# Performance work log

Measured on AMD Instinct MI355X. Metric: run time of the kernel, lower is better.

Reference implementation:

```python
import jax, jax.numpy as jnp
import numpy as np
from jax import lax

ANCHOR_BASE = np.array([
    [-37.254833, -82.50967, 53.254833, 98.50967],
    [-82.50967, -173.01933, 98.50967, 189.01933],
    [-173.01933, -354.03867, 189.01933, 370.03867],
    [-56.0, -56.0, 72.0, 72.0],
    [-120.0, -120.0, 136.0, 136.0],
    [-248.0, -248.0, 264.0, 264.0],
    [-82.50967, -37.254833, 98.50967, 53.254833],
    [-173.01933, -82.50967, 189.01933, 98.50967],
    [-354.03867, -173.01933, 370.03867, 189.01933]], dtype=np.float32)
FEAT_STRIDE = 16
IMG_H, IMG_W = 608, 800          # feature map 38x50 at stride 16
NMS_THRESH = 0.7
PRE_NMS, POST_NMS = 6000, 300
MIN_SIZE = 16.0                  # scale = 1.0


def setup_inputs() -> dict:
    key = jax.random.key(0)
    ks = jax.random.split(key, 7)
    H, W = 38, 50
    x = jax.random.normal(ks[0], (1, 512, H, W), jnp.float32)
    conv1_w = jax.random.normal(ks[1], (512, 512, 3, 3), jnp.float32) * 0.01
    conv1_b = jnp.zeros((512,), jnp.float32)
    loc_w = jax.random.normal(ks[2], (36, 512, 1, 1), jnp.float32) * 0.01
    loc_b = jnp.zeros((36,), jnp.float32)
    score_w = jax.random.normal(ks[3], (18, 512, 1, 1), jnp.float32) * 0.01
    score_b = jnp.zeros((18,), jnp.float32)
    return {"x": x, "conv1_w": conv1_w, "conv1_b": conv1_b,
            "loc_w": loc_w, "loc_b": loc_b,
            "score_w": score_w, "score_b": score_b}


def _conv(x, w, b, pad):
    y = lax.conv_general_dilated(x, w, (1, 1), pad,
                                 dimension_numbers=("NCHW", "OIHW", "NCHW"))
    return y + b[None, :, None, None]


def _make_anchors(h, w):
    ab = jnp.asarray(ANCHOR_BASE)                       # [A,4]
    yy = jnp.arange(h, dtype=jnp.float32) * FEAT_STRIDE
    xx = jnp.arange(w, dtype=jnp.float32) * FEAT_STRIDE
    sy, sx = jnp.meshgrid(yy, xx, indexing="ij")        # [h,w]
    shift = jnp.stack([sy, sx, sy, sx], axis=-1).reshape(-1, 4)  # [K,4]
    return (shift[:, None, :] + ab[None, :, :]).reshape(-1, 4)   # [K*A,4]


def _loc2bbox(anchor, loc):
    ah = anchor[:, 2] - anchor[:, 0]
    aw = anchor[:, 3] - anchor[:, 1]
    acy = anchor[:, 0] + 0.5 * ah
    acx = anchor[:, 1] + 0.5 * aw
    dy, dx, dh, dw = loc[:, 0], loc[:, 1], loc[:, 2], loc[:, 3]
    cy = dy * ah + acy
    cx = dx * aw + acx
    h = jnp.exp(dh) * ah
    w = jnp.exp(dw) * aw
    return jnp.stack([cy - 0.5 * h, cx - 0.5 * w,
                      cy + 0.5 * h, cx + 0.5 * w], axis=1)


def _iou_matrix(b):  # b: [K,4] (y1,x1,y2,x2)
    area = (b[:, 2] - b[:, 0]) * (b[:, 3] - b[:, 1])
    ty1 = jnp.maximum(b[:, None, 0], b[None, :, 0])
    tx1 = jnp.maximum(b[:, None, 1], b[None, :, 1])
    ty2 = jnp.minimum(b[:, None, 2], b[None, :, 2])
    tx2 = jnp.minimum(b[:, None, 3], b[None, :, 3])
    inter = jnp.clip(ty2 - ty1, 0) * jnp.clip(tx2 - tx1, 0)
    return inter / jnp.maximum(area[:, None] + area[None, :] - inter, 1e-9)


def _nms_keep(boxes, valid, thresh):
    # boxes already sorted by score desc; greedy suppression.
    K = boxes.shape[0]
    iou = _iou_matrix(boxes)                 # [K,K]
    idx = jnp.arange(K)

    def body(i, keep):
        sup = (iou[i] > thresh) & (idx > i) & keep[i]
        return keep & ~sup

    keep = lax.fori_loop(0, K, body, valid)
    return keep


def reference(x, conv1_w, conv1_b, loc_w, loc_b, score_w, score_b):
    H, W = x.shape[2], x.shape[3]
    A = ANCHOR_BASE.shape[0]

    h1 = jax.nn.relu(_conv(x, conv1_w, conv1_b, ((1, 1), (1, 1))))
    locs = _conv(h1, loc_w, loc_b, ((0, 0), (0, 0)))      # [1,36,H,W]
    scores = _conv(h1, score_w, score_b, ((0, 0), (0, 0)))  # [1,18,H,W]

    locs = locs.transpose(0, 2, 3, 1).reshape(-1, 4)        # [H*W*A,4]
    fg = scores.transpose(0, 2, 3, 1).reshape(H, W, A, 2)[..., 1].reshape(-1)

    anchor = _make_anchors(H, W)
    roi = _loc2bbox(anchor, locs)
    roi = jnp.stack([jnp.clip(roi[:, 0], 0, IMG_H),
                     jnp.clip(roi[:, 1], 0, IMG_W),
                     jnp.clip(roi[:, 2], 0, IMG_H),
                     jnp.clip(roi[:, 3], 0, IMG_W)], axis=1)

    hs = roi[:, 2] - roi[:, 0]
    ws = roi[:, 3] - roi[:, 1]
    valid = (hs >= MIN_SIZE) & (ws >= MIN_SIZE)
    score_f = jnp.where(valid, fg, -jnp.inf)

    top_scores, top_idx = lax.top_k(score_f, PRE_NMS)
    top_boxes = roi[top_idx]                                # [PRE_NMS,4]
    top_valid = top_scores > -jnp.inf

    keep = _nms_keep(top_boxes, top_valid, NMS_THRESH)

    # take first POST_NMS kept boxes into a fixed-shape output
    rank = jnp.cumsum(keep.astype(jnp.int32)) - 1
    dest = jnp.where(keep & (rank < POST_NMS), rank, POST_NMS)
    out = jnp.zeros((POST_NMS + 1, 4), top_boxes.dtype).at[dest].add(top_boxes)
    return out[:POST_NMS]
```

## Files before the change

### kernel.cpp

```cpp
#include <hip/hip_runtime.h>
#include <cstdint>
#include <cstddef>

typedef unsigned long long u64;

#define CIN   512
#define H     38
#define W     50
#define HW    1900
#define PH    40
#define PW    52
#define NA    17100
#define NSORT 32768
#define PRE   6000
#define POST  300
#define NW    94
#define MTS   6016

__constant__ float c_AB[36] = {
  -37.254833f,  -82.50967f,   53.254833f,  98.50967f,
  -82.50967f,  -173.01933f,   98.50967f,  189.01933f,
 -173.01933f,  -354.03867f,  189.01933f,  370.03867f,
  -56.f, -56.f, 72.f, 72.f,
 -120.f,-120.f,136.f,136.f,
 -248.f,-248.f,264.f,264.f,
  -82.50967f,  -37.254833f,   98.50967f,  53.254833f,
 -173.01933f,  -82.50967f,   189.01933f,  98.50967f,
 -354.03867f, -173.01933f,   370.03867f, 189.01933f
};

__global__ __launch_bounds__(256) void pad_kernel(const float* __restrict__ x, float* __restrict__ xp) {
  int idx = blockIdx.x * 256 + threadIdx.x;
  int c   = idx / (PH * PW);
  int rem = idx - c * (PH * PW);
  int yy  = rem / PW;
  int xx  = rem - yy * PW;
  float v = 0.f;
  if (yy >= 1 && yy <= H && xx >= 1 && xx <= W)
    v = x[(size_t)c * HW + (yy - 1) * W + (xx - 1)];
  xp[idx] = v;
}

__global__ __launch_bounds__(256) void wtrans_kernel(const float* __restrict__ w1, float* __restrict__ wt) {
  __shared__ float tile[9][16][17];
  int o0 = blockIdx.x * 16, i0 = blockIdx.y * 16;
  int tx = threadIdx.x & 15, ty = threadIdx.x >> 4;
  #pragma unroll
  for (int r = 0; r < 9; ++r)
    tile[r][tx][ty] = w1[((size_t)(o0 + ty) * CIN + (i0 + tx)) * 9 + r];
  __syncthreads();
  #pragma unroll
  for (int r = 0; r < 9; ++r)
    wt[((size_t)r * CIN + i0 + ty) * CIN + o0 + tx] = tile[r][ty][tx];
}

__global__ __launch_bounds__(256) void wt2prep_kernel(const float* __restrict__ lw, const float* __restrict__ sw,
                                                      float* __restrict__ wt2) {
  int t = blockIdx.x * 256 + threadIdx.x;
  int k = t >> 6, o = t & 63;
  float v = 0.f;
  if (o < 36)      v = lw[o * CIN + k];
  else if (o < 54) v = sw[(o - 36) * CIN + k];
  wt2[t] = v;
}

__global__ __launch_bounds__(256) void conv_gemm_kernel(const float* __restrict__ wt, const float* __restrict__ xp,
                                                        float* __restrict__ part) {
  __shared__ __align__(16) float As[16][64];
  __shared__ __align__(16) float Bs[16][64];
  const int tid   = threadIdx.x;
  const int obase = blockIdx.x * 64;
  const int pbase = blockIdx.y * 64;
  const int split = blockIdx.z;
  const int kbeg = split * 1536, kend = kbeg + 1536;
  const int krow = tid >> 4;
  const int c4   = (tid & 15) * 4;
  const int to   = (tid & 15) * 4;
  const int tp   = (tid >> 4) * 4;
  float acc[4][4] = {};
  float av[4], bv[4];

  auto loadAB = [&](int k0) {
    int k = k0 + krow;
    const float* ap = &wt[(size_t)k * CIN + obase + c4];
    av[0] = ap[0]; av[1] = ap[1]; av[2] = ap[2]; av[3] = ap[3];
    int r = k >> 9;
    int i = k & 511;
    int ky = r / 3, kx = r - ky * 3;
    const float* xpi = &xp[(size_t)i * (PH * PW)];
    #pragma unroll
    for (int j = 0; j < 4; ++j) {
      int p = pbase + c4 + j;
      float v = 0.f;
      if (p < HW) {
        int y = p / W, xx = p - y * W;
        v = xpi[(y + ky) * PW + xx + kx];
      }
      bv[j] = v;
    }
  };

  loadAB(kbeg);
  for (int k0 = kbeg; k0 < kend; k0 += 16) {
    __syncthreads();
    *(float4*)&As[krow][c4] = make_float4(av[0], av[1], av[2], av[3]);
    *(float4*)&Bs[krow][c4] = make_float4(bv[0], bv[1], bv[2], bv[3]);
    __syncthreads();
    if (k0 + 16 < kend) loadAB(k0 + 16);
    #pragma unroll
    for (int kk = 0; kk < 16; ++kk) {
      float4 a4 = *(const float4*)&As[kk][to];
      float4 b4 = *(const float4*)&Bs[kk][tp];
      float ar[4] = {a4.x, a4.y, a4.z, a4.w};
      float br[4] = {b4.x, b4.y, b4.z, b4.w};
      #pragma unroll
      for (int ii = 0; ii < 4; ++ii)
        #pragma unroll
        for (int jj = 0; jj < 4; ++jj)
          acc[ii][jj] += ar[ii] * br[jj];
    }
  }
  float* dst = part + (size_t)split * CIN * HW;
  #pragma unroll
  for (int ii = 0; ii < 4; ++ii) {
    int o = obase + to + ii;
    int p = pbase + tp;
    float* rowp = dst + (size_t)o * HW;
    if (p + 3 < HW) {
      *(float4*)&rowp[p] = make_float4(acc[ii][0], acc[ii][1], acc[ii][2], acc[ii][3]);
    } else {
      #pragma unroll
      for (int jj = 0; jj < 4; ++jj) if (p + jj < HW) rowp[p + jj] = acc[ii][jj];
    }
  }
}

__global__ __launch_bounds__(256) void reduce_relu_kernel(const float* __restrict__ part, const float* __restrict__ b1,
                                                          float* __restrict__ h1) {
  int idx = blockIdx.x * 256 + threadIdx.x;
  int o = idx / HW;
  float v = part[idx] + part[(size_t)CIN * HW + idx] + part[(size_t)2 * CIN * HW + idx] + b1[o];
  h1[idx] = v > 0.f ? v : 0.f;
}

__global__ __launch_bounds__(256) void heads_gemm_kernel(const float* __restrict__ wt2, const float* __restrict__ h1,
                                                         const float* __restrict__ lb, const float* __restrict__ sb,
                                                         float* __restrict__ c2) {
  __shared__ __align__(16) float As[16][64];
  __shared__ __align__(16) float Bs[16][64];
  const int tid   = threadIdx.x;
  const int pbase = blockIdx.x * 64;
  const int krow = tid >> 4;
  const int c4   = (tid & 15) * 4;
  const int to   = (tid & 15) * 4;
  const int tp   = (tid >> 4) * 4;
  float acc[4][4] = {};
  float av[4], bv[4];

  auto loadAB = [&](int k0) {
    int k = k0 + krow;
    const float4 a4 = *(const float4*)&wt2[k * 64 + c4];
    av[0] = a4.x; av[1] = a4.y; av[2] = a4.z; av[3] = a4.w;
    #pragma unroll
    for (int j = 0; j < 4; ++j) {
      int p = pbase + c4 + j;
      bv[j] = (p < HW) ? h1[(size_t)k * HW + p] : 0.f;
    }
  };

  loadAB(0);
  for (int k0 = 0; k0 < CIN; k0 += 16) {
    __syncthreads();
    *(float4*)&As[krow][c4] = make_float4(av[0], av[1], av[2], av[3]);
    *(float4*)&Bs[krow][c4] = make_float4(bv[0], bv[1], bv[2], bv[3]);
    __syncthreads();
    if (k0 + 16 < CIN) loadAB(k0 + 16);
    #pragma unroll
    for (int kk = 0; kk < 16; ++kk) {
      float4 a4 = *(const float4*)&As[kk][to];
      float4 b4 = *(const float4*)&Bs[kk][tp];
      float ar[4] = {a4.x, a4.y, a4.z, a4.w};
      float br[4] = {b4.x, b4.y, b4.z, b4.w};
      #pragma unroll
      for (int ii = 0; ii < 4; ++ii)
        #pragma unroll
        for (int jj = 0; jj < 4; ++jj)
          acc[ii][jj] += ar[ii] * br[jj];
    }
  }
  #pragma unroll
  for (int ii = 0; ii < 4; ++ii) {
    int o = to + ii;
    float bias = 0.f;
    if (o < 36) bias = lb[o]; else if (o < 54) bias = sb[o - 36];
    int p = pbase + tp;
    float* rowp = c2 + (size_t)o * HW;
    #pragma unroll
    for (int jj = 0; jj < 4; ++jj) if (p + jj < HW) rowp[p + jj] = acc[ii][jj] + bias;
  }
}

__global__ __launch_bounds__(256) void decode_kernel(const float* __restrict__ c2, float* __restrict__ roi,
                                                     u64* __restrict__ keys) {
  int n = blockIdx.x * 256 + threadIdx.x;
  if (n >= NSORT) return;
  if (n >= NA) { keys[n] = ~0ull; return; }
  unsigned p = (unsigned)n / 9u;
  unsigned a = (unsigned)n - p * 9u;
  unsigned y = p / 50u;
  unsigned x = p - y * 50u;
  float dy = c2[(a * 4 + 0) * HW + p];
  float dx = c2[(a * 4 + 1) * HW + p];
  float dh = c2[(a * 4 + 2) * HW + p];
  float dw = c2[(a * 4 + 3) * HW + p];
  float fg = c2[(37 + a * 2) * HW + p];
  float sy = (float)(y * 16u), sx = (float)(x * 16u);
  float ay1 = sy + c_AB[a * 4 + 0], ax1 = sx + c_AB[a * 4 + 1];
  float ay2 = sy + c_AB[a * 4 + 2], ax2 = sx + c_AB[a * 4 + 3];
  float ahh = ay2 - ay1, aww = ax2 - ax1;
  float acy = ay1 + 0.5f * ahh, acx = ax1 + 0.5f * aww;
  float cy = dy * ahh + acy, cx = dx * aww + acx;
  float hh = expf(dh) * ahh, ww = expf(dw) * aww;
  float y1 = cy - 0.5f * hh, x1 = cx - 0.5f * ww;
  float y2 = cy + 0.5f * hh, x2 = cx + 0.5f * ww;
  y1 = fminf(fmaxf(y1, 0.f), 608.f); x1 = fminf(fmaxf(x1, 0.f), 800.f);
  y2 = fminf(fmaxf(y2, 0.f), 608.f); x2 = fminf(fmaxf(x2, 0.f), 800.f);
  *(float4*)&roi[(size_t)n * 4] = make_float4(y1, x1, y2, x2);
  bool valid = ((y2 - y1) >= 16.f) && ((x2 - x1) >= 16.f);
  float sc = valid ? fg : -__builtin_huge_valf();
  unsigned m = __float_as_uint(sc);
  m = (m & 0x80000000u) ? ~m : (m | 0x80000000u);
  unsigned km = ~m;
  keys[n] = ((u64)km << 32) | (unsigned)n;
}

__global__ __launch_bounds__(1024) void sort_kernel(u64* __restrict__ keys) {
  __shared__ u64 s[8192];
  const int tid = threadIdx.x;
  u64* base = keys + (size_t)blockIdx.x * 8192;
  for (int i = tid; i < 8192; i += 1024) s[i] = base[i];
  __syncthreads();
  for (int k = 2; k <= 8192; k <<= 1) {
    for (int j = k >> 1; j > 0; j >>= 1) {
      for (int i = tid; i < 8192; i += 1024) {
        int l = i ^ j;
        if (l > i) {
          u64 xa = s[i], xb = s[l];
          bool up = ((i & k) == 0);
          if ((xa > xb) == up) { s[i] = xb; s[l] = xa; }
        }
      }
      __syncthreads();
    }
  }
  for (int i = tid; i < 8192; i += 1024) base[i] = s[i];
}

__device__ inline void merge_path(const u64* __restrict__ A, int nA, const u64* __restrict__ B, int nB,
                                  u64* __restrict__ dst, int d0, int cnt, int outLimit) {
  if (d0 >= outLimit || d0 >= nA + nB) return;
  int lo = d0 > nB ? d0 - nB : 0;
  int hi = d0 < nA ? d0 : nA;
  while (lo < hi) {
    int mid = (lo + hi) >> 1;
    if (A[mid] <= B[d0 - 1 - mid]) lo = mid + 1; else hi = mid;
  }
  int i = lo, j = d0 - lo;
  int end = d0 + cnt;
  if (end > nA + nB) end = nA + nB;
  if (end > outLimit) end = outLimit;
  for (int q = d0; q < end; ++q) {
    u64 v;
    if (i < nA && (j >= nB || A[i] <= B[j])) v = A[i++]; else v = B[j++];
    dst[q] = v;
  }
}
__global__ __launch_bounds__(256) void merge1_kernel(const u64* __restrict__ keys, u64* __restrict__ tmp) {
  int pair = blockIdx.y;
  int gid = blockIdx.x * 256 + threadIdx.x;
  const u64* A = keys + (size_t)pair * 16384;
  merge_path(A, 8192, A + 8192, 8192, tmp + (size_t)pair * 16384, gid * 16, 16, 16384);
}
__global__ __launch_bounds__(256) void merge2_kernel(const u64* __restrict__ tmp, u64* __restrict__ topk) {
  int gid = blockIdx.x * 256 + threadIdx.x;
  merge_path(tmp, 16384, tmp + 16384, 16384, topk, gid * 16, 16, 6016);
}

__global__ __launch_bounds__(256) void gather_kernel(const u64* __restrict__ topk, const float* __restrict__ roi,
                                                     float* __restrict__ tb, float* __restrict__ areaArr,
                                                     u64* __restrict__ valw) {
  int j = blockIdx.x * 256 + threadIdx.x;
  u64 key = (j < 6016) ? topk[j] : ~0ull;
  bool valid = (j < PRE) && ((unsigned)(key >> 32) < 0xFF800000u);
  if (j < PRE) {
    unsigned idx = (unsigned)key;
    float4 b = *(const float4*)&roi[(size_t)idx * 4];
    *(float4*)&tb[(size_t)j * 4] = b;
    areaArr[j] = (b.z - b.x) * (b.w - b.y);
  }
  u64 mask = __ballot(valid);
  if ((threadIdx.x & 63) == 0) {
    int wi = j >> 6;
    if (wi < NW) valw[wi] = mask;
  }
}

__global__ __launch_bounds__(256) void mask_kernel(const float* __restrict__ tb, const float* __restrict__ areaArr,
                                                   u64* __restrict__ MT) {
  int linear = blockIdx.x * 256 + threadIdx.x;
  if (linear >= NW * PRE) return;
  int w = linear / PRE;
  int i = linear - w * PRE;
  u64 bits = 0;
  int jbase = w * 64;
  if (jbase + 63 > i) {
    float4 bi = *(const float4*)&tb[(size_t)i * 4];
    float ai = areaArr[i];
    int jend = jbase + 64; if (jend > PRE) jend = PRE;
    int jst = jbase > i + 1 ? jbase : i + 1;
    for (int j = jst; j < jend; ++j) {
      float4 bj = *(const float4*)&tb[(size_t)j * 4];
      float ty1 = fmaxf(bi.x, bj.x);
      float tx1 = fmaxf(bi.y, bj.y);
      float ty2 = fminf(bi.z, bj.z);
      float tx2 = fminf(bi.w, bj.w);
      float ih = ty2 - ty1; if (ih < 0.f) ih = 0.f;
      float iw = tx2 - tx1; if (iw < 0.f) iw = 0.f;
      float inter = ih * iw;
      float denom = ai + areaArr[j] - inter;
      if (denom < 1e-9f) denom = 1e-9f;
      if (inter / denom > 0.7f) bits |= (1ull << (j - jbase));
    }
  }
  MT[(size_t)w * MTS + i] = bits;
}

__device__ inline u64 shfl_u64(u64 v, int src) {
  int lo = __shfl((int)(unsigned)(v & 0xffffffffull), src, 64);
  int hi = __shfl((int)(unsigned)(v >> 32), src, 64);
  return ((u64)(unsigned)hi << 32) | (unsigned)lo;
}

__global__ __launch_bounds__(64) void nms_scan_kernel(const u64* __restrict__ MT, const u64* __restrict__ valw,
                                                      const float* __restrict__ tb, float* __restrict__ out) {
  __shared__ u64 removed[NW];
  __shared__ int keepids[POST];
  const int lane = threadIdx.x;
  for (int wk = lane; wk < NW; wk += 64) removed[wk] = 0;
  __syncthreads();
  int kept = 0;
  bool done = false;
  for (int g = 0; g < NW && !done; ++g) {
    int row = g * 64 + lane;
    u64 cur = (row < PRE) ? MT[(size_t)g * MTS + row] : 0ull;
    u64 v = valw[g];
    u64 r = removed[g];
    u64 kb = 0;
    u64 remaining = v & ~r;
    while (remaining) {
      int c = __builtin_ctzll(remaining);
      if (lane == 0) keepids[kept] = g * 64 + c;
      kb |= (1ull << c);
      ++kept;
      if (kept >= POST) { done = true; break; }
      u64 cw = shfl_u64(cur, c);
      r |= cw;
      u64 above = (c == 63) ? 0ull : (~0ull << (c + 1));
      remaining = v & ~r & above;
    }
    if (!done) {
      __syncthreads();
      for (int wk = g + 1 + lane; wk < NW; wk += 64) {
        u64 acc2 = removed[wk];
        u64 m = kb;
        while (m) {
          int b = __builtin_ctzll(m); m &= m - 1;
          acc2 |= MT[(size_t)wk * MTS + g * 64 + b];
        }
        removed[wk] = acc2;
      }
      __syncthreads();
    }
  }
  __syncthreads();
  int kmax = kept < POST ? kept : POST;
  for (int rr = lane; rr < kmax; rr += 64) {
    float4 b = *(const float4*)&tb[(size_t)keepids[rr] * 4];
    *(float4*)&out[(size_t)rr * 4] = b;
  }
}

extern "C" void kernel_launch(void* const* d_in, const int* in_sizes, int n_in,
                              void* d_out, int out_size, void* d_ws, size_t ws_size,
                              hipStream_t stream) {
  (void)in_sizes; (void)n_in; (void)ws_size;
  const float* x  = (const float*)d_in[0];
  const float* w1 = (const float*)d_in[1];
  const float* b1 = (const float*)d_in[2];
  const float* lw = (const float*)d_in[3];
  const float* lb = (const float*)d_in[4];
  const float* sw = (const float*)d_in[5];
  const float* sb = (const float*)d_in[6];
  float* out = (float*)d_out;

  char* wp = (char*)d_ws;
  auto alloc = [&](size_t b) -> void* { void* p = wp; wp += (b + 255) & ~(size_t)255; return p; };
  float* xp      = (float*)alloc((size_t)CIN * PH * PW * 4);
  float* wt      = (float*)alloc((size_t)4608 * CIN * 4);
  float* part    = (float*)alloc((size_t)3 * CIN * HW * 4);
  float* h1      = (float*)alloc((size_t)CIN * HW * 4);
  float* wt2     = (float*)alloc((size_t)CIN * 64 * 4);
  float* c2      = (float*)alloc((size_t)64 * HW * 4);
  float* roi     = (float*)alloc((size_t)NA * 4 * 4);
  u64*   keys    = (u64*)alloc((size_t)NSORT * 8);
  u64*   tmp     = (u64*)alloc((size_t)NSORT * 8);
  u64*   topk    = (u64*)alloc((size_t)8192 * 8);
  float* tb      = (float*)alloc((size_t)PRE * 4 * 4);
  float* areaArr = (float*)alloc((size_t)PRE * 4);
  u64*   valw    = (u64*)alloc((size_t)NW * 8);
  u64*   MT      = (u64*)alloc((size_t)NW * MTS * 8);

  hipMemsetAsync(d_out, 0, (size_t)out_size * 4, stream);

  pad_kernel<<<(CIN * PH * PW) / 256, 256, 0, stream>>>(x, xp);
  wtrans_kernel<<<dim3(32, 32), 256, 0, stream>>>(w1, wt);
  wt2prep_kernel<<<(CIN * 64) / 256, 256, 0, stream>>>(lw, sw, wt2);
  conv_gemm_kernel<<<dim3(8, 30, 3), 256, 0, stream>>>(wt, xp, part);
  reduce_relu_kernel<<<(CIN * HW) / 256, 256, 0, stream>>>(part, b1, h1);
  heads_gemm_kernel<<<30, 256, 0, stream>>>(wt2, h1, lb, sb, c2);
  decode_kernel<<<NSORT / 256, 256, 0, stream>>>(c2, roi, keys);
  sort_kernel<<<4, 1024, 0, stream>>>(keys);
  merge1_kernel<<<dim3(4, 2), 256, 0, stream>>>(keys, tmp);
  merge2_kernel<<<2, 256, 0, stream>>>(tmp, topk);
  gather_kernel<<<24, 256, 0, stream>>>(topk, roi, tb, areaArr, valw);
  mask_kernel<<<(NW * PRE + 255) / 256, 256, 0, stream>>>(tb, areaArr, MT);
  nms_scan_kernel<<<1, 64, 0, stream>>>(MT, valw, tb, out);
}
```

Baseline: 561.3 us.

## Fuse prep kernels, enlarge conv GEMM tile, fuse heads+decode, shrink sort, restructure NMS

Merges the pad, weight-transpose, head-weight prep and key-padding kernels into one launch. Raises the conv GEMM tile to 128x128 with 8x8 per-thread accumulators and precomputed pixel offsets. Fuses the head GEMM with anchor decoding through shared memory, and shrinks the sort to 5 chunks of 4096 followed by a three-stage merge. Folds the gather step into the mask kernel using shared j-boxes, and replaces the NMS removed-mask update with a wave OR-reduction. This removes launches and global traffic, but the larger conv tile gives fewer blocks (180) and higher register pressure.

Result: slower. 783.1 us (+39.5%).

```diff
diff --git a/kernel.cpp b/kernel.cpp
--- a/kernel.cpp
+++ b/kernel.cpp
@@ -10,12 +10,23 @@
 #define HW    1900
 #define PH    40
 #define PW    52
+#define XPL   (PH*PW)
 #define NA    17100
-#define NSORT 32768
+#define NSORT 20480
+#define CHUNK 4096
 #define PRE   6000
 #define POST  300
 #define NW    94
 #define MTS   6016
+#define TOPN  6016
+#define KSPLIT 3
+#define KRANGE 1536
+
+#define PB_PAD    0
+#define PB_WT     4160
+#define PB_WT2    5184
+#define PB_KEY    5312
+#define PB_END    5325
 
 __constant__ float c_AB[36] = {
   -37.254833f,  -82.50967f,   53.254833f,  98.50967f,
@@ -29,50 +40,146 @@
  -354.03867f, -173.01933f,   370.03867f, 189.01933f
 };
 
-__global__ __launch_bounds__(256) void pad_kernel(const float* __restrict__ x, float* __restrict__ xp) {
+__global__ __launch_bounds__(256) void prep_kernel(const float* __restrict__ x, float* __restrict__ xp,
+                                                   const float* __restrict__ w1, float* __restrict__ wt,
+                                                   const float* __restrict__ lw, const float* __restrict__ sw,
+                                                   float* __restrict__ wt2, u64* __restrict__ keys) {
+  __shared__ float tile[9][16][17];
+  int bx = blockIdx.x;
+  int tid = threadIdx.x;
+  if (bx < PB_WT) {
+    int idx = bx * 256 + tid;
+    int c   = idx / XPL;
+    int rem = idx - c * XPL;
+    int yy  = rem / PW;
+    int xx  = rem - yy * PW;
+    float v = 0.f;
+    if (yy >= 1 && yy <= H && xx >= 1 && xx <= W)
+      v = x[(size_t)c * HW + (yy - 1) * W + (xx - 1)];
+    xp[idx] = v;
+  } else if (bx < PB_WT2) {
+    int b2 = bx - PB_WT;
+    int o0 = (b2 & 31) * 16, i0 = (b2 >> 5) * 16;
+    int tx = tid & 15, ty = tid >> 4;
+    #pragma unroll
+    for (int r = 0; r < 9; ++r)
+      tile[r][tx][ty] = w1[((size_t)(o0 + ty) * CIN + (i0 + tx)) * 9 + r];
+    __syncthreads();
+    #pragma unroll
+    for (int r = 0; r < 9; ++r)
+      wt[((size_t)r * CIN + i0 + ty) * CIN + o0 + tx] = tile[r][ty][tx];
+  } else if (bx < PB_KEY) {
+    int t = (bx - PB_WT2) * 256 + tid;
+    int k = t >> 6, o = t & 63;
+    float v = 0.f;
+    if (o < 36)      v = lw[o * CIN + k];
+    else if (o < 54) v = sw[(o - 36) * CIN + k];
+    wt2[t] = v;
+  } else {
+    int idx = (bx - PB_KEY) * 256 + tid;
+    int n = 17280 + idx;
+    if (n < NSORT) keys[n] = ~0ull;
+  }
+}
+
+__global__ __launch_bounds__(256, 1) void conv_gemm_kernel(const float* __restrict__ wt, const float* __restrict__ xp,
+                                                           float* __restrict__ part) {
+  __shared__ __align__(16) float As[16][128];
+  __shared__ __align__(16) float Bs[16][128];
+  const int tid   = threadIdx.x;
+  const int obase = blockIdx.x * 128;
+  const int pbase = blockIdx.y * 128;
+  const int split = blockIdx.z;
+  const int kbeg = split * KRANGE, kend = kbeg + KRANGE;
+
+  const int ar = tid >> 4;
+  const int ac = (tid & 15) * 8;
+  const int wave = tid >> 6, lane = tid & 63;
+  const int o_off = (wave & 1) * 64 + (lane & 7) * 8;
+  const int p_off = (wave >> 1) * 64 + (lane >> 3) * 8;
+
+  int poff[8]; int pok = 0;
+  #pragma unroll
+  for (int j = 0; j < 8; ++j) {
+    int p = pbase + ac + j;
+    int py = p / W, px = p - py * W;
+    poff[j] = py * PW + px;
+    if (p < HW) pok |= (1 << j);
+  }
+
+  float acc[8][8] = {};
+  float av[8], bv[8];
+
+  auto loadAB = [&](int k0) {
+    int k = k0 + ar;
+    const float* ap = &wt[(size_t)k * CIN + obase + ac];
+    #pragma unroll
+    for (int j = 0; j < 8; ++j) av[j] = ap[j];
+    int i = k & 511;
+    int r = k >> 9;
+    int ky = r / 3, kx = r - ky * 3;
+    const float* bp = &xp[(size_t)i * XPL + ky * PW + kx];
+    #pragma unroll
+    for (int j = 0; j < 8; ++j)
+      bv[j] = (pok & (1 << j)) ? bp[poff[j]] : 0.f;
+  };
+
+  loadAB(kbeg);
+  for (int k0 = kbeg; k0 < kend; k0 += 16) {
+    __syncthreads();
+    *(float4*)&As[ar][ac]     = make_float4(av[0], av[1], av[2], av[3]);
+    *(float4*)&As[ar][ac + 4] = make_float4(av[4], av[5], av[6], av[7]);
+    *(float4*)&Bs[ar][ac]     = make_float4(bv[0], bv[1], bv[2], bv[3]);
+    *(float4*)&Bs[ar][ac + 4] = make_float4(bv[4], bv[5], bv[6], bv[7]);
+    __syncthreads();
+    if (k0 + 16 < kend) loadAB(k0 + 16);
+    #pragma unroll
+    for (int kk = 0; kk < 16; ++kk) {
+      float4 a0 = *(const float4*)&As[kk][o_off];
+      float4 a1 = *(const float4*)&As[kk][o_off + 4];
+      float4 b0 = *(const float4*)&Bs[kk][p_off];
+      float4 b1 = *(const float4*)&Bs[kk][p_off + 4];
+      float ax[8] = {a0.x, a0.y, a0.z, a0.w, a1.x, a1.y, a1.z, a1.w};
+      float bx[8] = {b0.x, b0.y, b0.z, b0.w, b1.x, b1.y, b1.z, b1.w};
+      #pragma unroll
+      for (int ii = 0; ii < 8; ++ii)
+        #pragma unroll
+        for (int jj = 0; jj < 8; ++jj)
+          acc[ii][jj] += ax[ii] * bx[jj];
+    }
+  }
+  float* dst = part + (size_t)split * CIN * HW;
+  int p0 = pbase + p_off;
+  #pragma unroll
+  for (int ii = 0; ii < 8; ++ii) {
+    int o = obase + o_off + ii;
+    float* rowp = dst + (size_t)o * HW + p0;
+    if (p0 + 7 < HW) {
+      *(float4*)&rowp[0] = make_float4(acc[ii][0], acc[ii][1], acc[ii][2], acc[ii][3]);
+      *(float4*)&rowp[4] = make_float4(acc[ii][4], acc[ii][5], acc[ii][6], acc[ii][7]);
+    } else {
+      #pragma unroll
+      for (int jj = 0; jj < 8; ++jj) if (p0 + jj < HW) rowp[jj] = acc[ii][jj];
+    }
+  }
+}
+
+__global__ __launch_bounds__(256) void reduce_relu_kernel(const float* __restrict__ part, const float* __restrict__ b1,
+                                                          float* __restrict__ h1) {
   int idx = blockIdx.x * 256 + threadIdx.x;
-  int c   = idx / (PH * PW);
-  int rem = idx - c * (PH * PW);
-  int yy  = rem / PW;
-  int xx  = rem - yy * PW;
-  float v = 0.f;
-  if (yy >= 1 && yy <= H && xx >= 1 && xx <= W)
-    v = x[(size_t)c * HW + (yy - 1) * W + (xx - 1)];
-  xp[idx] = v;
-}
-
-__global__ __launch_bounds__(256) void wtrans_kernel(const float* __restrict__ w1, float* __restrict__ wt) {
-  __shared__ float tile[9][16][17];
-  int o0 = blockIdx.x * 16, i0 = blockIdx.y * 16;
-  int tx = threadIdx.x & 15, ty = threadIdx.x >> 4;
-  #pragma unroll
-  for (int r = 0; r < 9; ++r)
-    tile[r][tx][ty] = w1[((size_t)(o0 + ty) * CIN + (i0 + tx)) * 9 + r];
-  __syncthreads();
-  #pragma unroll
-  for (int r = 0; r < 9; ++r)
-    wt[((size_t)r * CIN + i0 + ty) * CIN + o0 + tx] = tile[r][ty][tx];
-}
-
-__global__ __launch_bounds__(256) void wt2prep_kernel(const float* __restrict__ lw, const float* __restrict__ sw,
-                                                      float* __restrict__ wt2) {
-  int t = blockIdx.x * 256 + threadIdx.x;
-  int k = t >> 6, o = t & 63;
-  float v = 0.f;
-  if (o < 36)      v = lw[o * CIN + k];
-  else if (o < 54) v = sw[(o - 36) * CIN + k];
-  wt2[t] = v;
-}
-
-__global__ __launch_bounds__(256) void conv_gemm_kernel(const float* __restrict__ wt, const float* __restrict__ xp,
-                                                        float* __restrict__ part) {
+  int o = idx / HW;
+  float v = part[idx] + part[(size_t)CIN * HW + idx] + part[(size_t)2 * CIN * HW + idx] + b1[o];
+  h1[idx] = v > 0.f ? v : 0.f;
+}
+
+__global__ __launch_bounds__(256) void heads_decode_kernel(const float* __restrict__ wt2, const float* __restrict__ h1,
+                                                           const float* __restrict__ lb, const float* __restrict__ sb,
+                                                           float* __restrict__ roi, u64* __restrict__ keys) {
   __shared__ __align__(16) float As[16][64];
   __shared__ __align__(16) float Bs[16][64];
+  __shared__ float c2s[64][65];
   const int tid   = threadIdx.x;
-  const int obase = blockIdx.x * 64;
-  const int pbase = blockIdx.y * 64;
-  const int split = blockIdx.z;
-  const int kbeg = split * 1536, kend = kbeg + 1536;
+  const int pbase = blockIdx.x * 64;
   const int krow = tid >> 4;
   const int c4   = (tid & 15) * 4;
   const int to   = (tid & 15) * 4;
@@ -82,31 +189,22 @@
 
   auto loadAB = [&](int k0) {
     int k = k0 + krow;
-    const float* ap = &wt[(size_t)k * CIN + obase + c4];
-    av[0] = ap[0]; av[1] = ap[1]; av[2] = ap[2]; av[3] = ap[3];
-    int r = k >> 9;
-    int i = k & 511;
-    int ky = r / 3, kx = r - ky * 3;
-    const float* xpi = &xp[(size_t)i * (PH * PW)];
+    const float4 a4 = *(const float4*)&wt2[k * 64 + c4];
+    av[0] = a4.x; av[1] = a4.y; av[2] = a4.z; av[3] = a4.w;
     #pragma unroll
     for (int j = 0; j < 4; ++j) {
       int p = pbase + c4 + j;
-      float v = 0.f;
-      if (p < HW) {
-        int y = p / W, xx = p - y * W;
-        v = xpi[(y + ky) * PW + xx + kx];
-      }
-      bv[j] = v;
+      bv[j] = (p < HW) ? h1[(size_t)k * HW + p] : 0.f;
     }
   };
 
-  loadAB(kbeg);
-  for (int k0 = kbeg; k0 < kend; k0 += 16) {
+  loadAB(0);
+  for (int k0 = 0; k0 < CIN; k0 += 16) {
     __syncthreads();
     *(float4*)&As[krow][c4] = make_float4(av[0], av[1], av[2], av[3]);
     *(float4*)&Bs[krow][c4] = make_float4(bv[0], bv[1], bv[2], bv[3]);
     __syncthreads();
-    if (k0 + 16 < kend) loadAB(k0 + 16);
+    if (k0 + 16 < CIN) loadAB(k0 + 16);
     #pragma unroll
     for (int kk = 0; kk < 16; ++kk) {
       float4 a4 = *(const float4*)&As[kk][to];
@@ -120,140 +218,72 @@
           acc[ii][jj] += ar[ii] * br[jj];
     }
   }
-  float* dst = part + (size_t)split * CIN * HW;
-  #pragma unroll
-  for (int ii = 0; ii < 4; ++ii) {
-    int o = obase + to + ii;
-    int p = pbase + tp;
-    float* rowp = dst + (size_t)o * HW;
-    if (p + 3 < HW) {
-      *(float4*)&rowp[p] = make_float4(acc[ii][0], acc[ii][1], acc[ii][2], acc[ii][3]);
-    } else {
-      #pragma unroll
-      for (int jj = 0; jj < 4; ++jj) if (p + jj < HW) rowp[p + jj] = acc[ii][jj];
-    }
-  }
-}
-
-__global__ __launch_bounds__(256) void reduce_relu_kernel(const float* __restrict__ part, const float* __restrict__ b1,
-                                                          float* __restrict__ h1) {
-  int idx = blockIdx.x * 256 + threadIdx.x;
-  int o = idx / HW;
-  float v = part[idx] + part[(size_t)CIN * HW + idx] + part[(size_t)2 * CIN * HW + idx] + b1[o];
-  h1[idx] = v > 0.f ? v : 0.f;
-}
-
-__global__ __launch_bounds__(256) void heads_gemm_kernel(const float* __restrict__ wt2, const float* __restrict__ h1,
-                                                         const float* __restrict__ lb, const float* __restrict__ sb,
-                                                         float* __restrict__ c2) {
-  __shared__ __align__(16) float As[16][64];
-  __shared__ __align__(16) float Bs[16][64];
-  const int tid   = threadIdx.x;
-  const int pbase = blockIdx.x * 64;
-  const int krow = tid >> 4;
-  const int c4   = (tid & 15) * 4;
-  const int to   = (tid & 15) * 4;
-  const int tp   = (tid >> 4) * 4;
-  float acc[4][4] = {};
-  float av[4], bv[4];
-
-  auto loadAB = [&](int k0) {
-    int k = k0 + krow;
-    const float4 a4 = *(const float4*)&wt2[k * 64 + c4];
-    av[0] = a4.x; av[1] = a4.y; av[2] = a4.z; av[3] = a4.w;
-    #pragma unroll
-    for (int j = 0; j < 4; ++j) {
-      int p = pbase + c4 + j;
-      bv[j] = (p < HW) ? h1[(size_t)k * HW + p] : 0.f;
-    }
-  };
-
-  loadAB(0);
-  for (int k0 = 0; k0 < CIN; k0 += 16) {
-    __syncthreads();
-    *(float4*)&As[krow][c4] = make_float4(av[0], av[1], av[2], av[3]);
-    *(float4*)&Bs[krow][c4] = make_float4(bv[0], bv[1], bv[2], bv[3]);
-    __syncthreads();
-    if (k0 + 16 < CIN) loadAB(k0 + 16);
-    #pragma unroll
-    for (int kk = 0; kk < 16; ++kk) {
-      float4 a4 = *(const float4*)&As[kk][to];
-      float4 b4 = *(const float4*)&Bs[kk][tp];
-      float ar[4] = {a4.x, a4.y, a4.z, a4.w};
-      float br[4] = {b4.x, b4.y, b4.z, b4.w};
-      #pragma unroll
-      for (int ii = 0; ii < 4; ++ii)
-        #pragma unroll
-        for (int jj = 0; jj < 4; ++jj)
-          acc[ii][jj] += ar[ii] * br[jj];
-    }
-  }
   #pragma unroll
   for (int ii = 0; ii < 4; ++ii) {
     int o = to + ii;
     float bias = 0.f;
     if (o < 36) bias = lb[o]; else if (o < 54) bias = sb[o - 36];
-    int p = pbase + tp;
-    float* rowp = c2 + (size_t)o * HW;
-    #pragma unroll
-    for (int jj = 0; jj < 4; ++jj) if (p + jj < HW) rowp[p + jj] = acc[ii][jj] + bias;
-  }
-}
-
-__global__ __launch_bounds__(256) void decode_kernel(const float* __restrict__ c2, float* __restrict__ roi,
-                                                     u64* __restrict__ keys) {
-  int n = blockIdx.x * 256 + threadIdx.x;
-  if (n >= NSORT) return;
-  if (n >= NA) { keys[n] = ~0ull; return; }
-  unsigned p = (unsigned)n / 9u;
-  unsigned a = (unsigned)n - p * 9u;
-  unsigned y = p / 50u;
-  unsigned x = p - y * 50u;
-  float dy = c2[(a * 4 + 0) * HW + p];
-  float dx = c2[(a * 4 + 1) * HW + p];
-  float dh = c2[(a * 4 + 2) * HW + p];
-  float dw = c2[(a * 4 + 3) * HW + p];
-  float fg = c2[(37 + a * 2) * HW + p];
-  float sy = (float)(y * 16u), sx = (float)(x * 16u);
-  float ay1 = sy + c_AB[a * 4 + 0], ax1 = sx + c_AB[a * 4 + 1];
-  float ay2 = sy + c_AB[a * 4 + 2], ax2 = sx + c_AB[a * 4 + 3];
-  float ahh = ay2 - ay1, aww = ax2 - ax1;
-  float acy = ay1 + 0.5f * ahh, acx = ax1 + 0.5f * aww;
-  float cy = dy * ahh + acy, cx = dx * aww + acx;
-  float hh = expf(dh) * ahh, ww = expf(dw) * aww;
-  float y1 = cy - 0.5f * hh, x1 = cx - 0.5f * ww;
-  float y2 = cy + 0.5f * hh, x2 = cx + 0.5f * ww;
-  y1 = fminf(fmaxf(y1, 0.f), 608.f); x1 = fminf(fmaxf(x1, 0.f), 800.f);
-  y2 = fminf(fmaxf(y2, 0.f), 608.f); x2 = fminf(fmaxf(x2, 0.f), 800.f);
-  *(float4*)&roi[(size_t)n * 4] = make_float4(y1, x1, y2, x2);
-  bool valid = ((y2 - y1) >= 16.f) && ((x2 - x1) >= 16.f);
-  float sc = valid ? fg : -__builtin_huge_valf();
-  unsigned m = __float_as_uint(sc);
-  m = (m & 0x80000000u) ? ~m : (m | 0x80000000u);
-  unsigned km = ~m;
-  keys[n] = ((u64)km << 32) | (unsigned)n;
+    #pragma unroll
+    for (int jj = 0; jj < 4; ++jj)
+      c2s[o][tp + jj] = acc[ii][jj] + bias;
+  }
+  __syncthreads();
+  for (int t = tid; t < 576; t += 256) {
+    int pl = t / 9, a = t - pl * 9;
+    int p = pbase + pl;
+    int n = p * 9 + a;
+    if (p >= HW) { if (p < 1920) keys[n] = ~0ull; continue; }
+    unsigned y = (unsigned)p / 50u;
+    unsigned x = (unsigned)p - y * 50u;
+    float dy = c2s[a * 4 + 0][pl];
+    float dx = c2s[a * 4 + 1][pl];
+    float dh = c2s[a * 4 + 2][pl];
+    float dw = c2s[a * 4 + 3][pl];
+    float fg = c2s[37 + a * 2][pl];
+    float sy = (float)(y * 16u), sx = (float)(x * 16u);
+    float ay1 = sy + c_AB[a * 4 + 0], ax1 = sx + c_AB[a * 4 + 1];
+    float ay2 = sy + c_AB[a * 4 + 2], ax2 = sx + c_AB[a * 4 + 3];
+    float ahh = ay2 - ay1, aww = ax2 - ax1;
+    float acy = ay1 + 0.5f * ahh, acx = ax1 + 0.5f * aww;
+    float cy = dy * ahh + acy, cx = dx * aww + acx;
+    float hh = expf(dh) * ahh, ww = expf(dw) * aww;
+    float y1 = cy - 0.5f * hh, x1 = cx - 0.5f * ww;
+    float y2 = cy + 0.5f * hh, x2 = cx + 0.5f * ww;
+    y1 = fminf(fmaxf(y1, 0.f), 608.f); x1 = fminf(fmaxf(x1, 0.f), 800.f);
+    y2 = fminf(fmaxf(y2, 0.f), 608.f); x2 = fminf(fmaxf(x2, 0.f), 800.f);
+    *(float4*)&roi[(size_t)n * 4] = make_float4(y1, x1, y2, x2);
+    bool valid = ((y2 - y1) >= 16.f) && ((x2 - x1) >= 16.f);
+    float sc = valid ? fg : -__builtin_huge_valf();
+    unsigned m = __float_as_uint(sc);
+    m = (m & 0x80000000u) ? ~m : (m | 0x80000000u);
+    unsigned km = ~m;
+    keys[n] = ((u64)km << 32) | (unsigned)n;
+  }
 }
 
 __global__ __launch_bounds__(1024) void sort_kernel(u64* __restrict__ keys) {
-  __shared__ u64 s[8192];
+  __shared__ u64 s[CHUNK];
   const int tid = threadIdx.x;
-  u64* base = keys + (size_t)blockIdx.x * 8192;
-  for (int i = tid; i < 8192; i += 1024) s[i] = base[i];
+  u64* base = keys + (size_t)blockIdx.x * CHUNK;
+  #pragma unroll
+  for (int i = 0; i < 4; ++i) s[tid + i * 1024] = base[tid + i * 1024];
   __syncthreads();
-  for (int k = 2; k <= 8192; k <<= 1) {
+  for (int k = 2; k <= CHUNK; k <<= 1) {
     for (int j = k >> 1; j > 0; j >>= 1) {
-      for (int i = tid; i < 8192; i += 1024) {
-        int l = i ^ j;
-        if (l > i) {
-          u64 xa = s[i], xb = s[l];
-          bool up = ((i & k) == 0);
-          if ((xa > xb) == up) { s[i] = xb; s[l] = xa; }
-        }
+      #pragma unroll
+      for (int it = 0; it < 2; ++it) {
+        int t = tid + it * 1024;
+        int i = ((t & ~(j - 1)) << 1) | (t & (j - 1));
+        int l = i | j;
+        bool up = ((i & k) == 0);
+        u64 xa = s[i], xb = s[l];
+        if ((xa > xb) == up) { s[i] = xb; s[l] = xa; }
       }
       __syncthreads();
     }
   }
-  for (int i = tid; i < 8192; i += 1024) base[i] = s[i];
+  #pragma unroll
+  for (int i = 0; i < 4; ++i) base[tid + i * 1024] = s[tid + i * 1024];
 }
 
 __device__ inline void merge_path(const u64* __restrict__ A, int nA, const u64* __restrict__ B, int nB,
@@ -278,58 +308,61 @@
 __global__ __launch_bounds__(256) void merge1_kernel(const u64* __restrict__ keys, u64* __restrict__ tmp) {
   int pair = blockIdx.y;
   int gid = blockIdx.x * 256 + threadIdx.x;
-  const u64* A = keys + (size_t)pair * 16384;
-  merge_path(A, 8192, A + 8192, 8192, tmp + (size_t)pair * 16384, gid * 16, 16, 16384);
-}
-__global__ __launch_bounds__(256) void merge2_kernel(const u64* __restrict__ tmp, u64* __restrict__ topk) {
+  const u64* A = keys + (size_t)pair * 8192;
+  merge_path(A, CHUNK, A + CHUNK, CHUNK, tmp + (size_t)pair * 8192, gid * 16, 16, TOPN);
+}
+__global__ __launch_bounds__(256) void merge2_kernel(const u64* __restrict__ tmp, u64* __restrict__ tmp2) {
   int gid = blockIdx.x * 256 + threadIdx.x;
-  merge_path(tmp, 16384, tmp + 16384, 16384, topk, gid * 16, 16, 6016);
-}
-
-__global__ __launch_bounds__(256) void gather_kernel(const u64* __restrict__ topk, const float* __restrict__ roi,
-                                                     float* __restrict__ tb, float* __restrict__ areaArr,
-                                                     u64* __restrict__ valw) {
-  int j = blockIdx.x * 256 + threadIdx.x;
-  u64 key = (j < 6016) ? topk[j] : ~0ull;
-  bool valid = (j < PRE) && ((unsigned)(key >> 32) < 0xFF800000u);
-  if (j < PRE) {
+  merge_path(tmp, TOPN, tmp + 8192, TOPN, tmp2, gid * 16, 16, TOPN);
+}
+__global__ __launch_bounds__(256) void merge3_kernel(const u64* __restrict__ tmp2, const u64* __restrict__ keys,
+                                                     u64* __restrict__ topk) {
+  int gid = blockIdx.x * 256 + threadIdx.x;
+  merge_path(tmp2, TOPN, keys + 16384, CHUNK, topk, gid * 16, 16, TOPN);
+}
+
+__global__ __launch_bounds__(256) void mask_kernel(const u64* __restrict__ topk, const float* __restrict__ roi,
+                                                   u64* __restrict__ MT, u64* __restrict__ valw) {
+  __shared__ float jy1[64], jx1[64], jy2[64], jx2[64], jar[64];
+  int w = blockIdx.x;
+  int tid = threadIdx.x;
+  if (tid < 64) {
+    int jj = w * 64 + tid;
+    u64 key = (jj < TOPN) ? topk[jj] : ~0ull;
     unsigned idx = (unsigned)key;
-    float4 b = *(const float4*)&roi[(size_t)idx * 4];
-    *(float4*)&tb[(size_t)j * 4] = b;
-    areaArr[j] = (b.z - b.x) * (b.w - b.y);
-  }
-  u64 mask = __ballot(valid);
-  if ((threadIdx.x & 63) == 0) {
-    int wi = j >> 6;
-    if (wi < NW) valw[wi] = mask;
-  }
-}
-
-__global__ __launch_bounds__(256) void mask_kernel(const float* __restrict__ tb, const float* __restrict__ areaArr,
-                                                   u64* __restrict__ MT) {
-  int linear = blockIdx.x * 256 + threadIdx.x;
-  if (linear >= NW * PRE) return;
-  int w = linear / PRE;
-  int i = linear - w * PRE;
+    float4 b = make_float4(0.f, 0.f, 0.f, 0.f);
+    if (idx < NA) b = *(const float4*)&roi[(size_t)idx * 4];
+    jy1[tid] = b.x; jx1[tid] = b.y; jy2[tid] = b.z; jx2[tid] = b.w;
+    jar[tid] = (b.z - b.x) * (b.w - b.y);
+    bool jv = (jj < PRE) && ((unsigned)(key >> 32) < 0xFF800000u);
+    u64 mvote = __ballot(jv);
+    if (tid == 0 && blockIdx.y == 0) valw[w] = mvote;
+  }
+  __syncthreads();
+  int i = blockIdx.y * 256 + tid;
+  if (i >= MTS) return;
   u64 bits = 0;
-  int jbase = w * 64;
-  if (jbase + 63 > i) {
-    float4 bi = *(const float4*)&tb[(size_t)i * 4];
-    float ai = areaArr[i];
+  if (i < PRE) {
+    u64 ikey = topk[i];
+    unsigned iidx = (unsigned)ikey;
+    float4 bi = make_float4(0.f, 0.f, 0.f, 0.f);
+    if (iidx < NA) bi = *(const float4*)&roi[(size_t)iidx * 4];
+    float ai = (bi.z - bi.x) * (bi.w - bi.y);
+    int jbase = w * 64;
     int jend = jbase + 64; if (jend > PRE) jend = PRE;
     int jst = jbase > i + 1 ? jbase : i + 1;
     for (int j = jst; j < jend; ++j) {
-      float4 bj = *(const float4*)&tb[(size_t)j * 4];
-      float ty1 = fmaxf(bi.x, bj.x);
-      float tx1 = fmaxf(bi.y, bj.y);
-      float ty2 = fminf(bi.z, bj.z);
-      float tx2 = fminf(bi.w, bj.w);
+      int jl = j - jbase;
+      float ty1 = fmaxf(bi.x, jy1[jl]);
+      float tx1 = fmaxf(bi.y, jx1[jl]);
+      float ty2 = fminf(bi.z, jy2[jl]);
+      float tx2 = fminf(bi.w, jx2[jl]);
       float ih = ty2 - ty1; if (ih < 0.f) ih = 0.f;
       float iw = tx2 - tx1; if (iw < 0.f) iw = 0.f;
       float inter = ih * iw;
-      float denom = ai + areaArr[j] - inter;
+      float denom = ai + jar[jl] - inter;
       if (denom < 1e-9f) denom = 1e-9f;
-      if (inter / denom > 0.7f) bits |= (1ull << (j - jbase));
+      if (inter / denom > 0.7f) bits |= (1ull << jl);
     }
   }
   MT[(size_t)w * MTS + i] = bits;
@@ -340,9 +373,19 @@
   int hi = __shfl((int)(unsigned)(v >> 32), src, 64);
   return ((u64)(unsigned)hi << 32) | (unsigned)lo;
 }
+__device__ inline u64 wave_or_u64(u64 x) {
+  #pragma unroll
+  for (int d = 1; d < 64; d <<= 1) {
+    int lo = __shfl_xor((int)(unsigned)(x & 0xffffffffull), d, 64);
+    int hi = __shfl_xor((int)(x >> 32), d, 64);
+    x |= ((u64)(unsigned)hi << 32) | (unsigned)lo;
+  }
+  return x;
+}
 
 __global__ __launch_bounds__(64) void nms_scan_kernel(const u64* __restrict__ MT, const u64* __restrict__ valw,
-                                                      const float* __restrict__ tb, float* __restrict__ out) {
+                                                      const u64* __restrict__ topk, const float* __restrict__ roi,
+                                                      float* __restrict__ out) {
   __shared__ u64 removed[NW];
   __shared__ int keepids[POST];
   const int lane = threadIdx.x;
@@ -352,40 +395,35 @@
   bool done = false;
   for (int g = 0; g < NW && !done; ++g) {
     int row = g * 64 + lane;
-    u64 cur = (row < PRE) ? MT[(size_t)g * MTS + row] : 0ull;
-    u64 v = valw[g];
-    u64 r = removed[g];
+    u64 cur = MT[(size_t)g * MTS + row];
+    u64 v = valw[g] & ~removed[g];
     u64 kb = 0;
-    u64 remaining = v & ~r;
-    while (remaining) {
-      int c = __builtin_ctzll(remaining);
+    while (v) {
+      int c = __builtin_ctzll(v);
       if (lane == 0) keepids[kept] = g * 64 + c;
       kb |= (1ull << c);
       ++kept;
       if (kept >= POST) { done = true; break; }
       u64 cw = shfl_u64(cur, c);
-      r |= cw;
+      v &= ~cw;
       u64 above = (c == 63) ? 0ull : (~0ull << (c + 1));
-      remaining = v & ~r & above;
-    }
-    if (!done) {
-      __syncthreads();
-      for (int wk = g + 1 + lane; wk < NW; wk += 64) {
-        u64 acc2 = removed[wk];
-        u64 m = kb;
-        while (m) {
-          int b = __builtin_ctzll(m); m &= m - 1;
-          acc2 |= MT[(size_t)wk * MTS + g * 64 + b];
-        }
-        removed[wk] = acc2;
+      v &= above;
+    }
+    if (!done && kb) {
+      for (int wk = g + 1; wk < NW; ++wk) {
+        u64 x = MT[(size_t)wk * MTS + g * 64 + lane];
+        if (!((kb >> lane) & 1ull)) x = 0;
+        x = wave_or_u64(x);
+        if (lane == 0) removed[wk] |= x;
       }
-      __syncthreads();
-    }
+    }
+    __syncthreads();
   }
   __syncthreads();
   int kmax = kept < POST ? kept : POST;
   for (int rr = lane; rr < kmax; rr += 64) {
-    float4 b = *(const float4*)&tb[(size_t)keepids[rr] * 4];
+    unsigned idx = (unsigned)topk[keepids[rr]];
+    float4 b = *(const float4*)&roi[(size_t)idx * 4];
     *(float4*)&out[(size_t)rr * 4] = b;
   }
 }
@@ -405,34 +443,28 @@
 
   char* wp = (char*)d_ws;
   auto alloc = [&](size_t b) -> void* { void* p = wp; wp += (b + 255) & ~(size_t)255; return p; };
-  float* xp      = (float*)alloc((size_t)CIN * PH * PW * 4);
-  float* wt      = (float*)alloc((size_t)4608 * CIN * 4);
-  float* part    = (float*)alloc((size_t)3 * CIN * HW * 4);
-  float* h1      = (float*)alloc((size_t)CIN * HW * 4);
-  float* wt2     = (float*)alloc((size_t)CIN * 64 * 4);
-  float* c2      = (float*)alloc((size_t)64 * HW * 4);
-  float* roi     = (float*)alloc((size_t)NA * 4 * 4);
-  u64*   keys    = (u64*)alloc((size_t)NSORT * 8);
-  u64*   tmp     = (u64*)alloc((size_t)NSORT * 8);
-  u64*   topk    = (u64*)alloc((size_t)8192 * 8);
-  float* tb      = (float*)alloc((size_t)PRE * 4 * 4);
-  float* areaArr = (float*)alloc((size_t)PRE * 4);
-  u64*   valw    = (u64*)alloc((size_t)NW * 8);
-  u64*   MT      = (u64*)alloc((size_t)NW * MTS * 8);
+  float* xp   = (float*)alloc((size_t)CIN * XPL * 4);
+  float* wt   = (float*)alloc((size_t)4608 * CIN * 4);
+  float* part = (float*)alloc((size_t)KSPLIT * CIN * HW * 4);
+  float* h1   = (float*)alloc((size_t)CIN * HW * 4);
+  float* wt2  = (float*)alloc((size_t)CIN * 64 * 4);
+  float* roi  = (float*)alloc((size_t)NA * 4 * 4);
+  u64*   keys = (u64*)alloc((size_t)NSORT * 8);
+  u64*   tmp  = (u64*)alloc((size_t)24576 * 8);
+  u64*   topk = (u64*)alloc((size_t)TOPN * 8);
+  u64*   valw = (u64*)alloc((size_t)NW * 8);
+  u64*   MT   = (u64*)alloc((size_t)NW * MTS * 8);
 
   hipMemsetAsync(d_out, 0, (size_t)out_size * 4, stream);
 
-  pad_kernel<<<(CIN * PH * PW) / 256, 256, 0, stream>>>(x, xp);
-  wtrans_kernel<<<dim3(32, 32), 256, 0, stream>>>(w1, wt);
-  wt2prep_kernel<<<(CIN * 64) / 256, 256, 0, stream>>>(lw, sw, wt2);
-  conv_gemm_kernel<<<dim3(8, 30, 3), 256, 0, stream>>>(wt, xp, part);
+  prep_kernel<<<PB_END, 256, 0, stream>>>(x, xp, w1, wt, lw, sw, wt2, keys);
+  conv_gemm_kernel<<<dim3(4, 15, KSPLIT), 256, 0, stream>>>(wt, xp, part);
   reduce_relu_kernel<<<(CIN * HW) / 256, 256, 0, stream>>>(part, b1, h1);
-  heads_gemm_kernel<<<30, 256, 0, stream>>>(wt2, h1, lb, sb, c2);
-  decode_kernel<<<NSORT / 256, 256, 0, stream>>>(c2, roi, keys);
-  sort_kernel<<<4, 1024, 0, stream>>>(keys);
-  merge1_kernel<<<dim3(4, 2), 256, 0, stream>>>(keys, tmp);
-  merge2_kernel<<<2, 256, 0, stream>>>(tmp, topk);
-  gather_kernel<<<24, 256, 0, stream>>>(topk, roi, tb, areaArr, valw);
-  mask_kernel<<<(NW * PRE + 255) / 256, 256, 0, stream>>>(tb, areaArr, MT);
-  nms_scan_kernel<<<1, 64, 0, stream>>>(MT, valw, tb, out);
-}
+  heads_decode_kernel<<<30, 256, 0, stream>>>(wt2, h1, lb, sb, roi, keys);
+  sort_kernel<<<5, 1024, 0, stream>>>(keys);
+  merge1_kernel<<<dim3(2, 2), 256, 0, stream>>>(keys, tmp);
+  merge2_kernel<<<2, 256, 0, stream>>>(tmp, tmp + 16384);
+  merge3_kernel<<<2, 256, 0, stream>>>(tmp + 16384, keys, topk);
+  mask_kernel<<<dim3(NW, 24), 256, 0, stream>>>(topk, roi, MT, valw);
+  nms_scan_kernel<<<1, 64, 0, stream>>>(MT, valw, topk, roi, out);
+}
```
